# Performance work log

Measured on AMD Instinct MI355X. Metric: run time of the kernel, lower is better.

## Reference

```python
import jax, jax.numpy as jnp
import numpy as np

N = 50000        # nodes
E = 800000       # edges (avg degree 16)
F = 64           # NUM_NODE_FEATURES == NUM_FILTERS
P = 32           # allocation.NUM_PHYS (policy logits per graph)
G = 64           # graphs in batch
MAX_DEG = 10     # PyG MFConv default max_degree


def setup_inputs() -> dict:
    key = jax.random.key(0)
    ks = jax.random.split(key, 12)
    x = jax.random.normal(ks[0], (N, F), jnp.float32)
    edge_index = jax.random.randint(ks[1], (2, E), 0, N, dtype=jnp.int32)
    batch = jnp.sort(jax.random.randint(ks[2], (N,), 0, G, dtype=jnp.int32))
    s = 1.0 / np.sqrt(F)
    return {
        "x": x,
        "edge_index": edge_index,
        "batch": batch,
        # GCNConv conv_in: F -> F
        "W_in": jax.random.normal(ks[3], (F, F), jnp.float32) * s,
        "b_in": jnp.zeros((F,), jnp.float32),
        # GCNConv conv_1: F -> F
        "W1": jax.random.normal(ks[4], (F, F), jnp.float32) * s,
        "b1": jnp.zeros((F,), jnp.float32),
        # MFConv conv_val: F -> 1, per-degree weights (deg 0..MAX_DEG)
        "Wl_val": jax.random.normal(ks[5], (MAX_DEG + 1, F, 1), jnp.float32) * s,
        "bl_val": jnp.zeros((MAX_DEG + 1, 1), jnp.float32),
        "Wr_val": jax.random.normal(ks[6], (MAX_DEG + 1, F, 1), jnp.float32) * s,
        # GCNConv conv_policy: F -> P
        "W_pol": jax.random.normal(ks[7], (F, P), jnp.float32) * s,
        "b_pol": jnp.zeros((P,), jnp.float32),
    }


def gcn_conv(x, edge_index, W, b):
    # PyG GCNConv: add self-loops, symmetric normalization, linear, scatter-add.
    src, dst = edge_index[0], edge_index[1]
    loop = jnp.arange(N, dtype=src.dtype)
    src = jnp.concatenate([src, loop])
    dst = jnp.concatenate([dst, loop])
    deg = jax.ops.segment_sum(jnp.ones_like(dst, x.dtype), dst, num_segments=N)
    dinv = jnp.where(deg > 0, jax.lax.rsqrt(deg), 0.0)
    norm = dinv[src] * dinv[dst]                 # [E+N]
    h = x @ W                                    # [N, out]
    out = jax.ops.segment_sum(norm[:, None] * h[src], dst, num_segments=N)
    return out + b


def mf_conv(x, edge_index, Wl, bl, Wr):
    # PyG MFConv: sum-aggregate neighbors, per-degree linear transforms.
    src, dst = edge_index[0], edge_index[1]
    h = jax.ops.segment_sum(x[src], dst, num_segments=N)     # neighbor sum [N,F]
    deg = jax.ops.segment_sum(jnp.ones((src.shape[0],), jnp.int32), dst, num_segments=N)
    deg = jnp.clip(deg, 0, MAX_DEG)                          # [N]
    # out = lins_l[deg](h) + lins_r[deg](x)  (lins_r has no bias)
    out = (jnp.einsum("nf,nfo->no", h, Wl[deg]) + bl[deg]
           + jnp.einsum("nf,nfo->no", x, Wr[deg]))
    return out


def reference(x, edge_index, batch, W_in, b_in, W1, b1, Wl_val, bl_val, Wr_val, W_pol, b_pol):
    h = gcn_conv(x, edge_index, W_in, b_in)
    h = gcn_conv(h, edge_index, W1, b1)
    val = mf_conv(h, edge_index, Wl_val, bl_val, Wr_val)          # [N,1]
    val = jax.ops.segment_sum(val, batch, num_segments=G)         # global_add_pool [G,1]
    pol = gcn_conv(h, edge_index, W_pol, b_pol)                   # [N,P]
    pol_sum = jax.ops.segment_sum(pol, batch, num_segments=G)
    cnt = jax.ops.segment_sum(jnp.ones((N,), x.dtype), batch, num_segments=G)
    pol = pol_sum / jnp.maximum(cnt, 1.0)[:, None]                # global_mean_pool [G,P]
    return (pol, val)
```

## Files before the change

kernel.cpp:

```cpp
#include <hip/hip_runtime.h>

#define F 64
#define P 32
#define MAXD 10
#define NGRP 8

__global__ void k_count_deg(const int* __restrict__ dst, int* __restrict__ deg, int E, int N) {
  int r = blockIdx.x & (NGRP - 1);
  float scale = (float)NGRP / (float)N;
  int gblk = blockIdx.x >> 3;
  int i = gblk * blockDim.x + threadIdx.x;
  int stride = (gridDim.x >> 3) * blockDim.x;
  int E4 = E >> 2;
  const int4* d4p = (const int4*)dst;
  for (int e4 = i; e4 < E4; e4 += stride) {
    int4 d4 = d4p[e4];
    int rr;
    rr = min(NGRP - 1, (int)((float)d4.x * scale)); if (rr == r) atomicAdd(&deg[d4.x], 1);
    rr = min(NGRP - 1, (int)((float)d4.y * scale)); if (rr == r) atomicAdd(&deg[d4.y], 1);
    rr = min(NGRP - 1, (int)((float)d4.z * scale)); if (rr == r) atomicAdd(&deg[d4.z], 1);
    rr = min(NGRP - 1, (int)((float)d4.w * scale)); if (rr == r) atomicAdd(&deg[d4.w], 1);
  }
  for (int e = (E & ~3) + i; e < E; e += stride) {
    int d = dst[e];
    int rr = min(NGRP - 1, (int)((float)d * scale));
    if (rr == r) atomicAdd(&deg[d], 1);
  }
}

__global__ void k_bsum(const int* __restrict__ deg, int* __restrict__ bsum, int N) {
  __shared__ int s[256];
  int t = threadIdx.x;
  int n = blockIdx.x * 256 + t;
  s[t] = (n < N) ? deg[n] : 0;
  __syncthreads();
  for (int o = 128; o > 0; o >>= 1) {
    if (t < o) s[t] += s[t + o];
    __syncthreads();
  }
  if (t == 0) bsum[blockIdx.x] = s[0];
}

__global__ void k_scan_bsum(int* __restrict__ bsum, int B) {
  __shared__ int s[1024];
  int t = threadIdx.x;
  int v = (t < B) ? bsum[t] : 0;
  s[t] = v;
  __syncthreads();
  for (int o = 1; o < 1024; o <<= 1) {
    int u = (t >= o) ? s[t - o] : 0;
    __syncthreads();
    s[t] += u;
    __syncthreads();
  }
  if (t < B) bsum[t] = s[t] - v;
}

__global__ void k_scan_fin(const int* __restrict__ deg, const int* __restrict__ bsum,
                           int* __restrict__ off, int* __restrict__ cur,
                           float* __restrict__ dinv, int N) {
  __shared__ int s[256];
  int t = threadIdx.x;
  int n = blockIdx.x * 256 + t;
  int v = (n < N) ? deg[n] : 0;
  s[t] = v;
  __syncthreads();
  for (int o = 1; o < 256; o <<= 1) {
    int u = (t >= o) ? s[t - o] : 0;
    __syncthreads();
    s[t] += u;
    __syncthreads();
  }
  if (n < N) {
    int ex = bsum[blockIdx.x] + s[t] - v;
    off[n] = ex;
    cur[n] = ex;
    dinv[n] = rsqrtf((float)(v + 1));
    if (n == N - 1) off[N] = ex + v;
  }
}

__global__ void k_fill(const int* __restrict__ src, const int* __restrict__ dst,
                       int* __restrict__ cur, int* __restrict__ csr, int E, int N) {
  int r = blockIdx.x & (NGRP - 1);
  float scale = (float)NGRP / (float)N;
  int gblk = blockIdx.x >> 3;
  int i = gblk * blockDim.x + threadIdx.x;
  int stride = (gridDim.x >> 3) * blockDim.x;
  int E4 = E >> 2;
  const int4* d4p = (const int4*)dst;
  for (int e4 = i; e4 < E4; e4 += stride) {
    int4 d4 = d4p[e4];
    int e = e4 * 4;
    int rr;
    rr = min(NGRP - 1, (int)((float)d4.x * scale));
    if (rr == r) { int pos = atomicAdd(&cur[d4.x], 1); csr[pos] = src[e]; }
    rr = min(NGRP - 1, (int)((float)d4.y * scale));
    if (rr == r) { int pos = atomicAdd(&cur[d4.y], 1); csr[pos] = src[e + 1]; }
    rr = min(NGRP - 1, (int)((float)d4.z * scale));
    if (rr == r) { int pos = atomicAdd(&cur[d4.z], 1); csr[pos] = src[e + 2]; }
    rr = min(NGRP - 1, (int)((float)d4.w * scale));
    if (rr == r) { int pos = atomicAdd(&cur[d4.w], 1); csr[pos] = src[e + 3]; }
  }
  for (int e = (E & ~3) + i; e < E; e += stride) {
    int d = dst[e];
    int rr = min(NGRP - 1, (int)((float)d * scale));
    if (rr == r) { int pos = atomicAdd(&cur[d], 1); csr[pos] = src[e]; }
  }
}

__global__ void k_scale(const float* __restrict__ x, const float* __restrict__ dinv,
                        float* __restrict__ xs, int N) {
  int i = blockIdx.x * blockDim.x + threadIdx.x;
  int stride = gridDim.x * blockDim.x;
  int tot = N * (F / 4);
  const float4* x4 = (const float4*)x;
  float4* xs4 = (float4*)xs;
  for (int idx = i; idx < tot; idx += stride) {
    int n = idx >> 4;
    float d = dinv[n];
    float4 v = x4[idx];
    v.x *= d; v.y *= d; v.z *= d; v.w *= d;
    xs4[idx] = v;
  }
}

__device__ __forceinline__ float rdl(float4 v, int k) {
  float c = (k & 3) == 0 ? v.x : (k & 3) == 1 ? v.y : (k & 3) == 2 ? v.z : v.w;
  return __int_as_float(__builtin_amdgcn_readlane(__float_as_int(c), k >> 2));
}

template <bool WRITE_SCALED>
__global__ void k_gcn(const float* __restrict__ xs, const int* __restrict__ csr,
                      const int* __restrict__ off, const float* __restrict__ dinv,
                      const float* __restrict__ W, const float* __restrict__ bias,
                      float* __restrict__ out, int N) {
  constexpr int NPW = 4;
  int wid = (blockIdx.x * blockDim.x + threadIdx.x) >> 6;
  int lane = threadIdx.x & 63;
  int nwaves = (gridDim.x * blockDim.x) >> 6;
  int g = lane >> 4, l = lane & 15;
  float w[F];
#pragma unroll
  for (int k = 0; k < F; ++k) w[k] = W[k * F + lane];
  float bv = bias[lane];
  for (int base = wid * NPW; base < N; base += nwaves * NPW) {
#pragma unroll 1
    for (int ni = 0; ni < NPW; ++ni) {
      int n = base + ni;
      if (n >= N) break;
      int e0 = off[n], e1 = off[n + 1];
      float4 acc;
      if (g == 0)
        acc = *(const float4*)&xs[(size_t)n * F + l * 4];
      else
        acc = make_float4(0.f, 0.f, 0.f, 0.f);
      for (int e = e0; e < e1; e += 64) {
        int cnt = min(64, e1 - e);
        int se = (e + lane < e1) ? csr[e + lane] : -1;
        int nfull = cnt >> 4;
        int j = 0;
        for (int u = 0; u < nfull; ++u, j += 4) {
          int s0 = __shfl(se, (j + 0) * 4 + g, 64);
          int s1 = __shfl(se, (j + 1) * 4 + g, 64);
          int s2 = __shfl(se, (j + 2) * 4 + g, 64);
          int s3 = __shfl(se, (j + 3) * 4 + g, 64);
          float4 v0 = *(const float4*)&xs[(size_t)s0 * F + l * 4];
          float4 v1 = *(const float4*)&xs[(size_t)s1 * F + l * 4];
          float4 v2 = *(const float4*)&xs[(size_t)s2 * F + l * 4];
          float4 v3 = *(const float4*)&xs[(size_t)s3 * F + l * 4];
          acc.x += (v0.x + v1.x) + (v2.x + v3.x);
          acc.y += (v0.y + v1.y) + (v2.y + v3.y);
          acc.z += (v0.z + v1.z) + (v2.z + v3.z);
          acc.w += (v0.w + v1.w) + (v2.w + v3.w);
        }
        int nj = (cnt + 3) >> 2;
        for (; j < nj; ++j) {
          int s = __shfl(se, j * 4 + g, 64);
          if (s >= 0) {
            float4 v = *(const float4*)&xs[(size_t)s * F + l * 4];
            acc.x += v.x; acc.y += v.y; acc.z += v.z; acc.w += v.w;
          }
        }
      }
#pragma unroll
      for (int o = 16; o < 64; o <<= 1) {
        acc.x += __shfl_xor(acc.x, o, 64);
        acc.y += __shfl_xor(acc.y, o, 64);
        acc.z += __shfl_xor(acc.z, o, 64);
        acc.w += __shfl_xor(acc.w, o, 64);
      }
      float y0 = 0.f, y1 = 0.f, y2 = 0.f, y3 = 0.f;
#pragma unroll
      for (int k = 0; k < F; k += 4) {
        y0 += rdl(acc, k) * w[k];
        y1 += rdl(acc, k + 1) * w[k + 1];
        y2 += rdl(acc, k + 2) * w[k + 2];
        y3 += rdl(acc, k + 3) * w[k + 3];
      }
      float dn = dinv[n];
      float y = dn * ((y0 + y1) + (y2 + y3)) + bv;
      if (WRITE_SCALED) y *= dn;
      out[(size_t)n * F + lane] = y;
    }
  }
}

__global__ void k_mfpol(const float* __restrict__ H, const int* __restrict__ csr,
                        const int* __restrict__ off, const float* __restrict__ dinv,
                        const float* __restrict__ Wl, const float* __restrict__ bl,
                        const float* __restrict__ Wr, float* __restrict__ val,
                        float* __restrict__ u, int N) {
  int wave = (blockIdx.x * blockDim.x + threadIdx.x) >> 6;
  int lane = threadIdx.x & 63;
  if (wave >= N) return;
  int n = wave;
  int e0 = off[n], e1 = off[n + 1];
  int g = lane >> 4, l = lane & 15;
  float4 ah = make_float4(0.f, 0.f, 0.f, 0.f);
  float4 aw = make_float4(0.f, 0.f, 0.f, 0.f);
  for (int e = e0; e < e1; e += 64) {
    int cnt = min(64, e1 - e);
    int idx = e + lane;
    int se = (idx < e1) ? csr[idx] : -1;
    float dv = (se >= 0) ? dinv[se] : 0.f;
    int nfull = cnt >> 4;
    int j = 0;
    for (int uu = 0; uu < nfull; ++uu, j += 4) {
      int s0 = __shfl(se, (j + 0) * 4 + g, 64);
      int s1 = __shfl(se, (j + 1) * 4 + g, 64);
      int s2 = __shfl(se, (j + 2) * 4 + g, 64);
      int s3 = __shfl(se, (j + 3) * 4 + g, 64);
      float d0 = __shfl(dv, (j + 0) * 4 + g, 64);
      float d1 = __shfl(dv, (j + 1) * 4 + g, 64);
      float d2 = __shfl(dv, (j + 2) * 4 + g, 64);
      float d3 = __shfl(dv, (j + 3) * 4 + g, 64);
      float4 v0 = *(const float4*)&H[(size_t)s0 * F + l * 4];
      float4 v1 = *(const float4*)&H[(size_t)s1 * F + l * 4];
      float4 v2 = *(const float4*)&H[(size_t)s2 * F + l * 4];
      float4 v3 = *(const float4*)&H[(size_t)s3 * F + l * 4];
      ah.x += (v0.x + v1.x) + (v2.x + v3.x);
      ah.y += (v0.y + v1.y) + (v2.y + v3.y);
      ah.z += (v0.z + v1.z) + (v2.z + v3.z);
      ah.w += (v0.w + v1.w) + (v2.w + v3.w);
      aw.x += (d0 * v0.x + d1 * v1.x) + (d2 * v2.x + d3 * v3.x);
      aw.y += (d0 * v0.y + d1 * v1.y) + (d2 * v2.y + d3 * v3.y);
      aw.z += (d0 * v0.z + d1 * v1.z) + (d2 * v2.z + d3 * v3.z);
      aw.w += (d0 * v0.w + d1 * v1.w) + (d2 * v2.w + d3 * v3.w);
    }
    int nj = (cnt + 3) >> 2;
    for (; j < nj; ++j) {
      int sl = j * 4 + g;
      int s = __shfl(se, sl, 64);
      float dd = __shfl(dv, sl, 64);
      if (s >= 0) {
        float4 v = *(const float4*)&H[(size_t)s * F + l * 4];
        ah.x += v.x; ah.y += v.y; ah.z += v.z; ah.w += v.w;
        aw.x += dd * v.x; aw.y += dd * v.y; aw.z += dd * v.z; aw.w += dd * v.w;
      }
    }
  }
#pragma unroll
  for (int o = 16; o < 64; o <<= 1) {
    ah.x += __shfl_xor(ah.x, o, 64); ah.y += __shfl_xor(ah.y, o, 64);
    ah.z += __shfl_xor(ah.z, o, 64); ah.w += __shfl_xor(ah.w, o, 64);
    aw.x += __shfl_xor(aw.x, o, 64); aw.y += __shfl_xor(aw.y, o, 64);
    aw.z += __shfl_xor(aw.z, o, 64); aw.w += __shfl_xor(aw.w, o, 64);
  }
  int dc = min(e1 - e0, MAXD);
  float dn = dinv[n];
  float4 hn = *(const float4*)&H[(size_t)n * F + l * 4];
  float4 wl4 = *(const float4*)&Wl[dc * F + l * 4];
  float4 wr4 = *(const float4*)&Wr[dc * F + l * 4];
  float part = ah.x * wl4.x + ah.y * wl4.y + ah.z * wl4.z + ah.w * wl4.w
             + hn.x * wr4.x + hn.y * wr4.y + hn.z * wr4.z + hn.w * wr4.w;
#pragma unroll
  for (int o = 1; o < 16; o <<= 1) part += __shfl_xor(part, o, 64);
  if (lane == 0) val[n] = part + bl[dc];
  if (g == 0) {
    float4 r;
    r.x = (aw.x + dn * hn.x) * dn;
    r.y = (aw.y + dn * hn.y) * dn;
    r.z = (aw.z + dn * hn.z) * dn;
    r.w = (aw.w + dn * hn.w) * dn;
    *(float4*)&u[(size_t)n * F + l * 4] = r;
  }
}

__global__ void k_pool2(const float* __restrict__ u, const float* __restrict__ valn,
                        const int* __restrict__ batch, float* __restrict__ Uacc,
                        float* __restrict__ valg, float* __restrict__ cntg, int N) {
  __shared__ float Ul[64 * F];
  __shared__ float Vl[64], Cl[64];
  int t = threadIdx.x;
  for (int i = t; i < 64 * F; i += 256) Ul[i] = 0.f;
  if (t < 64) { Vl[t] = 0.f; Cl[t] = 0.f; }
  __syncthreads();
  int base = blockIdx.x * 256;
  int f = t & 63, r = t >> 6;
  for (int i = r; i < 256; i += 4) {
    int n = base + i;
    if (n >= N) break;
    int g = batch[n];
    atomicAdd(&Ul[g * F + f], u[(size_t)n * F + f]);
    if (f == 0) { atomicAdd(&Vl[g], valn[n]); atomicAdd(&Cl[g], 1.f); }
  }
  __syncthreads();
  int last = min(base + 256, N) - 1;
  if (last < base) return;
  int gmin = batch[base], gmax = batch[last];
  int ng = gmax - gmin + 1;
  for (int idx = t; idx < ng * F; idx += 256) {
    int g = gmin + (idx >> 6), ff = idx & 63;
    atomicAdd(&Uacc[g * F + ff], Ul[g * F + ff]);
  }
  for (int idx = t; idx < ng; idx += 256) {
    int g = gmin + idx;
    atomicAdd(&valg[g], Vl[g]);
    atomicAdd(&cntg[g], Cl[g]);
  }
}

__global__ void k_polfin(const float* __restrict__ Uacc, const float* __restrict__ valg,
                         const float* __restrict__ cntg, const float* __restrict__ W_pol,
                         const float* __restrict__ b_pol, float* __restrict__ out, int G) {
  int i = blockIdx.x * blockDim.x + threadIdx.x;
  if (i < G * P) {
    int g = i >> 5, p = i & 31;
    float s = 0.f;
#pragma unroll
    for (int k = 0; k < F; ++k) s += Uacc[g * F + k] * W_pol[k * P + p];
    out[i] = s / fmaxf(cntg[g], 1.f) + b_pol[p];
  }
  if (i < G) out[(size_t)G * P + i] = valg[i];
}

extern "C" void kernel_launch(void* const* d_in, const int* in_sizes, int n_in,
                              void* d_out, int out_size, void* d_ws, size_t ws_size,
                              hipStream_t stream) {
  const float* x = (const float*)d_in[0];
  const int* ei = (const int*)d_in[1];
  const int* batch = (const int*)d_in[2];
  const float* W_in = (const float*)d_in[3];
  const float* b_in = (const float*)d_in[4];
  const float* W1 = (const float*)d_in[5];
  const float* b1 = (const float*)d_in[6];
  const float* Wl = (const float*)d_in[7];
  const float* bl = (const float*)d_in[8];
  const float* Wr = (const float*)d_in[9];
  const float* W_pol = (const float*)d_in[10];
  const float* b_pol = (const float*)d_in[11];
  float* out = (float*)d_out;

  const int N = in_sizes[0] / F;
  const int E = in_sizes[1] / 2;
  const int G = out_size / (P + 1);
  const int* esrc = ei;
  const int* edst = ei + E;
  const int NB = (N + 255) / 256;

  char* ws = (char*)d_ws;
  size_t o = 0;
  auto alloc = [&](size_t bytes) {
    char* r = ws + o;
    o = (o + bytes + 255) & ~(size_t)255;
    return r;
  };
  char* zbase = ws;
  int* deg = (int*)alloc((size_t)N * 4);
  float* Uacc = (float*)alloc((size_t)G * F * 4);
  float* valg = (float*)alloc((size_t)G * 4);
  float* cntg = (float*)alloc((size_t)G * 4);
  size_t zbytes = o;
  int* off = (int*)alloc((size_t)(N + 1) * 4);
  int* cur = (int*)alloc((size_t)N * 4);
  float* dinv = (float*)alloc((size_t)N * 4);
  int* csr = (int*)alloc((size_t)E * 4);
  float* valn = (float*)alloc((size_t)N * 4);
  int* bsum = (int*)alloc(1024 * 4);
  float* bufA = (float*)alloc((size_t)N * F * 4);
  float* bufB = (float*)alloc((size_t)N * F * 4);
  (void)ws_size; (void)n_in;

  hipMemsetAsync(zbase, 0, zbytes, stream);

  const int bs = 256;
  k_count_deg<<<2048, bs, 0, stream>>>(edst, deg, E, N);
  k_bsum<<<NB, bs, 0, stream>>>(deg, bsum, N);
  k_scan_bsum<<<1, 1024, 0, stream>>>(bsum, NB);
  k_scan_fin<<<NB, bs, 0, stream>>>(deg, bsum, off, cur, dinv, N);
  k_fill<<<2048, bs, 0, stream>>>(esrc, edst, cur, csr, E, N);

  k_scale<<<2048, bs, 0, stream>>>(x, dinv, bufA, N);

  int gcnBlocks = 2048;
  k_gcn<true><<<gcnBlocks, bs, 0, stream>>>(bufA, csr, off, dinv, W_in, b_in, bufB, N);
  k_gcn<false><<<gcnBlocks, bs, 0, stream>>>(bufB, csr, off, dinv, W1, b1, bufA, N);

  int aggBlocks = (N * 64 + bs - 1) / bs;
  k_mfpol<<<aggBlocks, bs, 0, stream>>>(bufA, csr, off, dinv, Wl, bl, Wr, valn, bufB, N);

  int poolBlocks = (N + 255) / 256;
  k_pool2<<<poolBlocks, bs, 0, stream>>>(bufB, valn, batch, Uacc, valg, cntg, N);
  k_polfin<<<(G * P + bs - 1) / bs, bs, 0, stream>>>(Uacc, valg, cntg, W_pol, b_pol, out, G);
}
```

Measured before the change: 244.9 us.

## Process four nodes per wave with 16-lane groups in GCN and MF kernels

Restructures the GCN and MF/policy aggregation kernels so that each wavefront handles four nodes at once, one per 16-lane group, instead of spreading a single node's edges across all 64 lanes and reducing with cross-lane shuffles. This removes the per-node cross-group shuffle reduction and the mostly idle lanes when a node has few edges (average degree 16). It also launches enough blocks to cover every node in one pass. The cost is load imbalance inside a wave when the four nodes have different degrees, plus extra readlane work to feed the per-node matvec in the GCN kernel.

```diff
diff --git a/kernel.cpp b/kernel.cpp
--- a/kernel.cpp
+++ b/kernel.cpp
@@ -125,9 +125,8 @@
   }
 }
 
-__device__ __forceinline__ float rdl(float4 v, int k) {
-  float c = (k & 3) == 0 ? v.x : (k & 3) == 1 ? v.y : (k & 3) == 2 ? v.z : v.w;
-  return __int_as_float(__builtin_amdgcn_readlane(__float_as_int(c), k >> 2));
+__device__ __forceinline__ float rdlane(float v, int srclane) {
+  return __int_as_float(__builtin_amdgcn_readlane(__float_as_int(v), srclane));
 }
 
 template <bool WRITE_SCALED>
@@ -135,7 +134,6 @@
                       const int* __restrict__ off, const float* __restrict__ dinv,
                       const float* __restrict__ W, const float* __restrict__ bias,
                       float* __restrict__ out, int N) {
-  constexpr int NPW = 4;
   int wid = (blockIdx.x * blockDim.x + threadIdx.x) >> 6;
   int lane = threadIdx.x & 63;
   int nwaves = (gridDim.x * blockDim.x) >> 6;
@@ -144,64 +142,50 @@
 #pragma unroll
   for (int k = 0; k < F; ++k) w[k] = W[k * F + lane];
   float bv = bias[lane];
-  for (int base = wid * NPW; base < N; base += nwaves * NPW) {
-#pragma unroll 1
-    for (int ni = 0; ni < NPW; ++ni) {
-      int n = base + ni;
-      if (n >= N) break;
-      int e0 = off[n], e1 = off[n + 1];
-      float4 acc;
-      if (g == 0)
-        acc = *(const float4*)&xs[(size_t)n * F + l * 4];
-      else
-        acc = make_float4(0.f, 0.f, 0.f, 0.f);
-      for (int e = e0; e < e1; e += 64) {
-        int cnt = min(64, e1 - e);
-        int se = (e + lane < e1) ? csr[e + lane] : -1;
-        int nfull = cnt >> 4;
-        int j = 0;
-        for (int u = 0; u < nfull; ++u, j += 4) {
-          int s0 = __shfl(se, (j + 0) * 4 + g, 64);
-          int s1 = __shfl(se, (j + 1) * 4 + g, 64);
-          int s2 = __shfl(se, (j + 2) * 4 + g, 64);
-          int s3 = __shfl(se, (j + 3) * 4 + g, 64);
-          float4 v0 = *(const float4*)&xs[(size_t)s0 * F + l * 4];
-          float4 v1 = *(const float4*)&xs[(size_t)s1 * F + l * 4];
-          float4 v2 = *(const float4*)&xs[(size_t)s2 * F + l * 4];
-          float4 v3 = *(const float4*)&xs[(size_t)s3 * F + l * 4];
-          acc.x += (v0.x + v1.x) + (v2.x + v3.x);
-          acc.y += (v0.y + v1.y) + (v2.y + v3.y);
-          acc.z += (v0.z + v1.z) + (v2.z + v3.z);
-          acc.w += (v0.w + v1.w) + (v2.w + v3.w);
-        }
-        int nj = (cnt + 3) >> 2;
-        for (; j < nj; ++j) {
-          int s = __shfl(se, j * 4 + g, 64);
-          if (s >= 0) {
-            float4 v = *(const float4*)&xs[(size_t)s * F + l * 4];
-            acc.x += v.x; acc.y += v.y; acc.z += v.z; acc.w += v.w;
-          }
-        }
-      }
-#pragma unroll
-      for (int o = 16; o < 64; o <<= 1) {
-        acc.x += __shfl_xor(acc.x, o, 64);
-        acc.y += __shfl_xor(acc.y, o, 64);
-        acc.z += __shfl_xor(acc.z, o, 64);
-        acc.w += __shfl_xor(acc.w, o, 64);
-      }
+  for (int base = wid * 4; base < N; base += nwaves * 4) {
+    int n = min(base + g, N - 1);
+    int e0 = off[n], e1 = off[n + 1];
+    float dnode = dinv[n];
+    float4 acc = *(const float4*)&xs[(size_t)n * F + l * 4];
+    for (int win = e0; win < e1; win += 16) {
+      int m = min(16, e1 - win);
+      int ce = (win + l < e1) ? csr[win + l] : 0;
+      int j = 0;
+      for (; j + 4 <= m; j += 4) {
+        int s0 = __shfl(ce, g * 16 + j + 0, 64);
+        int s1 = __shfl(ce, g * 16 + j + 1, 64);
+        int s2 = __shfl(ce, g * 16 + j + 2, 64);
+        int s3 = __shfl(ce, g * 16 + j + 3, 64);
+        float4 v0 = *(const float4*)&xs[(size_t)s0 * F + l * 4];
+        float4 v1 = *(const float4*)&xs[(size_t)s1 * F + l * 4];
+        float4 v2 = *(const float4*)&xs[(size_t)s2 * F + l * 4];
+        float4 v3 = *(const float4*)&xs[(size_t)s3 * F + l * 4];
+        acc.x += (v0.x + v1.x) + (v2.x + v3.x);
+        acc.y += (v0.y + v1.y) + (v2.y + v3.y);
+        acc.z += (v0.z + v1.z) + (v2.z + v3.z);
+        acc.w += (v0.w + v1.w) + (v2.w + v3.w);
+      }
+      for (; j < m; ++j) {
+        int s = __shfl(ce, g * 16 + j, 64);
+        float4 v = *(const float4*)&xs[(size_t)s * F + l * 4];
+        acc.x += v.x; acc.y += v.y; acc.z += v.z; acc.w += v.w;
+      }
+    }
+#pragma unroll
+    for (int gg = 0; gg < 4; ++gg) {
       float y0 = 0.f, y1 = 0.f, y2 = 0.f, y3 = 0.f;
 #pragma unroll
       for (int k = 0; k < F; k += 4) {
-        y0 += rdl(acc, k) * w[k];
-        y1 += rdl(acc, k + 1) * w[k + 1];
-        y2 += rdl(acc, k + 2) * w[k + 2];
-        y3 += rdl(acc, k + 3) * w[k + 3];
-      }
-      float dn = dinv[n];
-      float y = dn * ((y0 + y1) + (y2 + y3)) + bv;
-      if (WRITE_SCALED) y *= dn;
-      out[(size_t)n * F + lane] = y;
+        y0 += rdlane(acc.x, gg * 16 + (k >> 2)) * w[k + 0];
+        y1 += rdlane(acc.y, gg * 16 + (k >> 2)) * w[k + 1];
+        y2 += rdlane(acc.z, gg * 16 + (k >> 2)) * w[k + 2];
+        y3 += rdlane(acc.w, gg * 16 + (k >> 2)) * w[k + 3];
+      }
+      float dd = rdlane(dnode, gg * 16);
+      float y = dd * ((y0 + y1) + (y2 + y3)) + bv;
+      if (WRITE_SCALED) y *= dd;
+      int nn = base + gg;
+      if (nn < N) out[(size_t)nn * F + lane] = y;
     }
   }
 }
@@ -211,79 +195,70 @@
                         const float* __restrict__ Wl, const float* __restrict__ bl,
                         const float* __restrict__ Wr, float* __restrict__ val,
                         float* __restrict__ u, int N) {
-  int wave = (blockIdx.x * blockDim.x + threadIdx.x) >> 6;
+  int wid = (blockIdx.x * blockDim.x + threadIdx.x) >> 6;
   int lane = threadIdx.x & 63;
-  if (wave >= N) return;
-  int n = wave;
-  int e0 = off[n], e1 = off[n + 1];
+  int nwaves = (gridDim.x * blockDim.x) >> 6;
   int g = lane >> 4, l = lane & 15;
-  float4 ah = make_float4(0.f, 0.f, 0.f, 0.f);
-  float4 aw = make_float4(0.f, 0.f, 0.f, 0.f);
-  for (int e = e0; e < e1; e += 64) {
-    int cnt = min(64, e1 - e);
-    int idx = e + lane;
-    int se = (idx < e1) ? csr[idx] : -1;
-    float dv = (se >= 0) ? dinv[se] : 0.f;
-    int nfull = cnt >> 4;
-    int j = 0;
-    for (int uu = 0; uu < nfull; ++uu, j += 4) {
-      int s0 = __shfl(se, (j + 0) * 4 + g, 64);
-      int s1 = __shfl(se, (j + 1) * 4 + g, 64);
-      int s2 = __shfl(se, (j + 2) * 4 + g, 64);
-      int s3 = __shfl(se, (j + 3) * 4 + g, 64);
-      float d0 = __shfl(dv, (j + 0) * 4 + g, 64);
-      float d1 = __shfl(dv, (j + 1) * 4 + g, 64);
-      float d2 = __shfl(dv, (j + 2) * 4 + g, 64);
-      float d3 = __shfl(dv, (j + 3) * 4 + g, 64);
-      float4 v0 = *(const float4*)&H[(size_t)s0 * F + l * 4];
-      float4 v1 = *(const float4*)&H[(size_t)s1 * F + l * 4];
-      float4 v2 = *(const float4*)&H[(size_t)s2 * F + l * 4];
-      float4 v3 = *(const float4*)&H[(size_t)s3 * F + l * 4];
-      ah.x += (v0.x + v1.x) + (v2.x + v3.x);
-      ah.y += (v0.y + v1.y) + (v2.y + v3.y);
-      ah.z += (v0.z + v1.z) + (v2.z + v3.z);
-      ah.w += (v0.w + v1.w) + (v2.w + v3.w);
-      aw.x += (d0 * v0.x + d1 * v1.x) + (d2 * v2.x + d3 * v3.x);
-      aw.y += (d0 * v0.y + d1 * v1.y) + (d2 * v2.y + d3 * v3.y);
-      aw.z += (d0 * v0.z + d1 * v1.z) + (d2 * v2.z + d3 * v3.z);
-      aw.w += (d0 * v0.w + d1 * v1.w) + (d2 * v2.w + d3 * v3.w);
-    }
-    int nj = (cnt + 3) >> 2;
-    for (; j < nj; ++j) {
-      int sl = j * 4 + g;
-      int s = __shfl(se, sl, 64);
-      float dd = __shfl(dv, sl, 64);
-      if (s >= 0) {
+  for (int base = wid * 4; base < N; base += nwaves * 4) {
+    bool valid = (base + g) < N;
+    int n = min(base + g, N - 1);
+    int e0 = off[n], e1 = off[n + 1];
+    float dn = dinv[n];
+    float4 ah = make_float4(0.f, 0.f, 0.f, 0.f);
+    float4 aw = make_float4(0.f, 0.f, 0.f, 0.f);
+    for (int win = e0; win < e1; win += 16) {
+      int m = min(16, e1 - win);
+      bool p = (win + l < e1);
+      int ce = p ? csr[win + l] : 0;
+      float cd = p ? dinv[ce] : 0.f;
+      int j = 0;
+      for (; j + 4 <= m; j += 4) {
+        int s0 = __shfl(ce, g * 16 + j + 0, 64);
+        int s1 = __shfl(ce, g * 16 + j + 1, 64);
+        int s2 = __shfl(ce, g * 16 + j + 2, 64);
+        int s3 = __shfl(ce, g * 16 + j + 3, 64);
+        float d0 = __shfl(cd, g * 16 + j + 0, 64);
+        float d1 = __shfl(cd, g * 16 + j + 1, 64);
+        float d2 = __shfl(cd, g * 16 + j + 2, 64);
+        float d3 = __shfl(cd, g * 16 + j + 3, 64);
+        float4 v0 = *(const float4*)&H[(size_t)s0 * F + l * 4];
+        float4 v1 = *(const float4*)&H[(size_t)s1 * F + l * 4];
+        float4 v2 = *(const float4*)&H[(size_t)s2 * F + l * 4];
+        float4 v3 = *(const float4*)&H[(size_t)s3 * F + l * 4];
+        ah.x += (v0.x + v1.x) + (v2.x + v3.x);
+        ah.y += (v0.y + v1.y) + (v2.y + v3.y);
+        ah.z += (v0.z + v1.z) + (v2.z + v3.z);
+        ah.w += (v0.w + v1.w) + (v2.w + v3.w);
+        aw.x += (d0 * v0.x + d1 * v1.x) + (d2 * v2.x + d3 * v3.x);
+        aw.y += (d0 * v0.y + d1 * v1.y) + (d2 * v2.y + d3 * v3.y);
+        aw.z += (d0 * v0.z + d1 * v1.z) + (d2 * v2.z + d3 * v3.z);
+        aw.w += (d0 * v0.w + d1 * v1.w) + (d2 * v2.w + d3 * v3.w);
+      }
+      for (; j < m; ++j) {
+        int s = __shfl(ce, g * 16 + j, 64);
+        float dd = __shfl(cd, g * 16 + j, 64);
         float4 v = *(const float4*)&H[(size_t)s * F + l * 4];
         ah.x += v.x; ah.y += v.y; ah.z += v.z; ah.w += v.w;
         aw.x += dd * v.x; aw.y += dd * v.y; aw.z += dd * v.z; aw.w += dd * v.w;
       }
     }
-  }
-#pragma unroll
-  for (int o = 16; o < 64; o <<= 1) {
-    ah.x += __shfl_xor(ah.x, o, 64); ah.y += __shfl_xor(ah.y, o, 64);
-    ah.z += __shfl_xor(ah.z, o, 64); ah.w += __shfl_xor(ah.w, o, 64);
-    aw.x += __shfl_xor(aw.x, o, 64); aw.y += __shfl_xor(aw.y, o, 64);
-    aw.z += __shfl_xor(aw.z, o, 64); aw.w += __shfl_xor(aw.w, o, 64);
-  }
-  int dc = min(e1 - e0, MAXD);
-  float dn = dinv[n];
-  float4 hn = *(const float4*)&H[(size_t)n * F + l * 4];
-  float4 wl4 = *(const float4*)&Wl[dc * F + l * 4];
-  float4 wr4 = *(const float4*)&Wr[dc * F + l * 4];
-  float part = ah.x * wl4.x + ah.y * wl4.y + ah.z * wl4.z + ah.w * wl4.w
-             + hn.x * wr4.x + hn.y * wr4.y + hn.z * wr4.z + hn.w * wr4.w;
-#pragma unroll
-  for (int o = 1; o < 16; o <<= 1) part += __shfl_xor(part, o, 64);
-  if (lane == 0) val[n] = part + bl[dc];
-  if (g == 0) {
-    float4 r;
-    r.x = (aw.x + dn * hn.x) * dn;
-    r.y = (aw.y + dn * hn.y) * dn;
-    r.z = (aw.z + dn * hn.z) * dn;
-    r.w = (aw.w + dn * hn.w) * dn;
-    *(float4*)&u[(size_t)n * F + l * 4] = r;
+    int dc = min(e1 - e0, MAXD);
+    float4 hn = *(const float4*)&H[(size_t)n * F + l * 4];
+    float4 wl4 = *(const float4*)&Wl[dc * F + l * 4];
+    float4 wr4 = *(const float4*)&Wr[dc * F + l * 4];
+    float part = ah.x * wl4.x + ah.y * wl4.y + ah.z * wl4.z + ah.w * wl4.w
+               + hn.x * wr4.x + hn.y * wr4.y + hn.z * wr4.z + hn.w * wr4.w;
+#pragma unroll
+    for (int o = 1; o < 16; o <<= 1) part += __shfl_xor(part, o, 64);
+    if (l == 0 && valid) val[n] = part + bl[dc];
+    if (valid) {
+      float4 r;
+      r.x = (aw.x + dn * hn.x) * dn;
+      r.y = (aw.y + dn * hn.y) * dn;
+      r.z = (aw.z + dn * hn.z) * dn;
+      r.w = (aw.w + dn * hn.w) * dn;
+      *(float4*)&u[(size_t)n * F + l * 4] = r;
+    }
   }
 }
 
@@ -393,12 +368,11 @@
 
   k_scale<<<2048, bs, 0, stream>>>(x, dinv, bufA, N);
 
-  int gcnBlocks = 2048;
-  k_gcn<true><<<gcnBlocks, bs, 0, stream>>>(bufA, csr, off, dinv, W_in, b_in, bufB, N);
-  k_gcn<false><<<gcnBlocks, bs, 0, stream>>>(bufB, csr, off, dinv, W1, b1, bufA, N);
-
-  int aggBlocks = (N * 64 + bs - 1) / bs;
-  k_mfpol<<<aggBlocks, bs, 0, stream>>>(bufA, csr, off, dinv, Wl, bl, Wr, valn, bufB, N);
+  int gBlocks = (N + 15) / 16;
+  k_gcn<true><<<gBlocks, bs, 0, stream>>>(bufA, csr, off, dinv, W_in, b_in, bufB, N);
+  k_gcn<false><<<gBlocks, bs, 0, stream>>>(bufB, csr, off, dinv, W1, b1, bufA, N);
+
+  k_mfpol<<<gBlocks, bs, 0, stream>>>(bufA, csr, off, dinv, Wl, bl, Wr, valn, bufB, N);
 
   int poolBlocks = (N + 255) / 256;
   k_pool2<<<poolBlocks, bs, 0, stream>>>(bufB, valn, batch, Uacc, valg, cntg, N);
```

New measurement: 235.6 us. 3.8% less time.
